# Kernel tuning notes

Hardware: AMD Instinct MI355X
Metric: run time of the kernel (lower is better)

## Reference

```python
import jax, jax.numpy as jnp
import numpy as np

N_NODES = 50000
N_EDGES = 600000
N_GRAPHS = 64
N_LAYERS = 4
D = 128
BN_EPS = 1e-5


def setup_inputs() -> dict:
    key = jax.random.key(0)
    ks = jax.random.split(key, 12)
    inp = {
        'x_node': jax.random.randint(ks[0], (N_NODES, 1), 0, 119, dtype=jnp.int64) if jax.config.jax_enable_x64 else jax.random.randint(ks[0], (N_NODES, 1), 0, 119).astype(jnp.int32),
        'edge_index': jax.random.randint(ks[1], (2, N_EDGES), 0, N_NODES).astype(jnp.int32),
        'batch': jnp.sort(jax.random.randint(ks[2], (N_NODES,), 0, N_GRAPHS)).astype(jnp.int32),
        'emb_table': jax.random.normal(ks[3], (119, D), jnp.float32),
        'conv_w1': jax.random.normal(ks[4], (N_LAYERS, D, D), jnp.float32) * 0.05,
        'conv_b1': jnp.zeros((N_LAYERS, D), jnp.float32),
        'bn1_g': jnp.ones((N_LAYERS, D), jnp.float32),
        'bn1_b': jnp.zeros((N_LAYERS, D), jnp.float32),
        'conv_w2': jax.random.normal(ks[5], (N_LAYERS, D, D), jnp.float32) * 0.05,
        'conv_b2': jnp.zeros((N_LAYERS, D), jnp.float32),
        'bn2_g': jnp.ones((N_LAYERS, D), jnp.float32),
        'bn2_b': jnp.zeros((N_LAYERS, D), jnp.float32),
        'lin1_w': jax.random.normal(ks[6], (D, 2 * D), jnp.float32) * 0.05,
        'lin1_b': jnp.zeros((2 * D,), jnp.float32),
        'lin2_w': jax.random.normal(ks[7], (2 * D, 10), jnp.float32) * 0.05,
        'lin2_b': jnp.zeros((10,), jnp.float32),
    }
    return inp


def _bn(h, g, b):
    # BatchNorm1d over the node axis (training-mode batch statistics, biased var)
    mu = jnp.mean(h, axis=0, keepdims=True)
    var = jnp.mean((h - mu) ** 2, axis=0, keepdims=True)
    return (h - mu) * jax.lax.rsqrt(var + BN_EPS) * g + b


def reference(x_node, edge_index, batch, emb_table, conv_w1, conv_b1, bn1_g, bn1_b,
              conv_w2, conv_b2, bn2_g, bn2_b, lin1_w, lin1_b, lin2_w, lin2_b):
    x = emb_table[x_node[:, 0]]                      # [N, D] node embedding
    src, dst = edge_index[0], edge_index[1]          # j, i in the torch code
    eps = 0.0
    for l in range(N_LAYERS):
        msg = x[src]                                 # gather x_j, [E, D]
        agg = jax.ops.segment_sum(msg, dst, num_segments=N_NODES)  # scatter-add to targets
        h = agg + (1.0 + eps) * x
        h = jax.nn.relu(_bn(h @ conv_w1[l] + conv_b1[l], bn1_g[l], bn1_b[l]))
        h = jax.nn.relu(_bn(h @ conv_w2[l] + conv_b2[l], bn2_g[l], bn2_b[l]))
        x = h
    # jump_mode=None -> last layer; readout: per-graph mean pooling
    ones = jnp.ones((N_NODES,), x.dtype)
    counts = jax.ops.segment_sum(ones, batch, num_segments=N_GRAPHS)
    pooled = jax.ops.segment_sum(x, batch, num_segments=N_GRAPHS)
    pooled = pooled / jnp.maximum(counts, 1.0)[:, None]             # [B, D]
    out = jax.nn.relu(pooled @ lin1_w + lin1_b)
    return out @ lin2_w + lin2_b                     # [B, 10]
```

## Files before the change

kernel.cpp:

```cpp
#include <hip/hip_runtime.h>
#include <hip/hip_fp16.h>

#define N_NODES 50000
#define N_EDGES 600000
#define N_GRAPHS 64
#define N_LAYERS 4
#define D 128
#define BN_EPS 1e-5f

#define SCAN_NB 49
#define GB 782

#define EMB_NB 6250
#define ZERO_NB 14
#define RPK_NB 8

typedef __attribute__((ext_vector_type(8))) short short8;
typedef __attribute__((ext_vector_type(8))) _Float16 half8;
typedef __attribute__((ext_vector_type(4))) float f32x4;

#define WLO_SCALE 2048.0f
#define WLO_INV (1.0f / 2048.0f)

__device__ __forceinline__ float half_bits_to_f32(short b) {
  union { unsigned short u; __half h; } cv;
  cv.u = (unsigned short)b;
  return __half2float(cv.h);
}
__device__ __forceinline__ unsigned short f32_to_half_bits(float f) {
  union { __half h; unsigned short u; } cv;
  cv.h = __float2half(f);
  return cv.u;
}

__global__ __launch_bounds__(256) void setup_kernel(const int* __restrict__ idx,
    const float* __restrict__ emb, __half* __restrict__ xh,
    int* __restrict__ counts, const float* __restrict__ cw1,
    const float* __restrict__ cw2, unsigned short* __restrict__ Wh,
    unsigned short* __restrict__ Wl) {
  int bb = blockIdx.x;
  int t = threadIdx.x;
  if (bb < EMB_NB) {
    int tid = bb * 256 + t;
    if (tid >= N_NODES * 32) return;
    int n = tid >> 5, c4 = tid & 31;
    int e = idx[n];
    float4 v = ((const float4*)emb)[(size_t)e * 32 + c4];
    __half2 a = __float22half2_rn(make_float2(v.x, v.y));
    __half2 b = __float22half2_rn(make_float2(v.z, v.w));
    ((__half2*)xh)[(size_t)tid * 2] = a;
    ((__half2*)xh)[(size_t)tid * 2 + 1] = b;
  } else if (bb < EMB_NB + ZERO_NB) {
    int tid = (bb - EMB_NB) * 256 + t;
    for (int i = tid; i < N_NODES; i += ZERO_NB * 256) counts[i] = 0;
  } else {
    int b = bb - (EMB_NB + ZERO_NB);
    int l = b >> 1, which = b & 1;
    const float* Wm = (which ? cw2 : cw1) + (size_t)l * D * D;
    unsigned short* outh = Wh + (size_t)b * D * D;
    unsigned short* outl = Wl + (size_t)b * D * D;
    for (int T = t; T < 2048; T += 256) {
      int ks = T >> 9, ct = (T >> 6) & 7, lane = T & 63;
      int kbase = ks * 32 + ((lane >> 4) << 3);
      int c = ct * 16 + (lane & 15);
      unsigned short hs[8], ls[8];
#pragma unroll
      for (int e = 0; e < 8; ++e) {
        float v = Wm[(size_t)(kbase + e) * D + c];
        __half hh = __float2half_rn(v);
        float rem = v - __half2float(hh);
        __half hl = __float2half_rn(rem * WLO_SCALE);
        union { __half h; unsigned short u; } c1, c2;
        c1.h = hh; c2.h = hl;
        hs[e] = c1.u;
        ls[e] = c2.u;
      }
      *(ushort4*)(outh + (size_t)T * 8)     = *(ushort4*)&hs[0];
      *(ushort4*)(outh + (size_t)T * 8 + 4) = *(ushort4*)&hs[4];
      *(ushort4*)(outl + (size_t)T * 8)     = *(ushort4*)&ls[0];
      *(ushort4*)(outl + (size_t)T * 8 + 4) = *(ushort4*)&ls[4];
    }
  }
}

__global__ __launch_bounds__(256) void count_kernel(const int* __restrict__ dst,
    int* __restrict__ counts) {
  int e = blockIdx.x * 256 + threadIdx.x;
  if (e < N_EDGES) atomicAdd(&counts[dst[e]], 1);
}

__global__ __launch_bounds__(256) void scan_block_kernel(const int* __restrict__ counts,
    int* __restrict__ offsets, int* __restrict__ partials) {
  __shared__ int s[256];
  int t = threadIdx.x;
  int base = blockIdx.x * 1024 + t * 4;
  int v[4];
#pragma unroll
  for (int i = 0; i < 4; ++i) v[i] = (base + i < N_NODES) ? counts[base + i] : 0;
  int tsum = v[0] + v[1] + v[2] + v[3];
  s[t] = tsum;
  __syncthreads();
  for (int off = 1; off < 256; off <<= 1) {
    int add = (t >= off) ? s[t - off] : 0;
    __syncthreads();
    s[t] += add;
    __syncthreads();
  }
  int run = s[t] - tsum;
#pragma unroll
  for (int i = 0; i < 4; ++i) {
    if (base + i < N_NODES) offsets[base + i] = run;
    run += v[i];
  }
  if (t == 255) partials[blockIdx.x] = s[255];
}

__global__ __launch_bounds__(256) void add_offsets_kernel(int* __restrict__ offsets,
    const int* __restrict__ partials, int* __restrict__ cursor) {
  __shared__ int pre[SCAN_NB];
  int t = threadIdx.x;
  if (t < SCAN_NB) pre[t] = partials[t];
  __syncthreads();
  if (t == 0) {
    int run = 0;
    for (int b = 0; b < SCAN_NB; ++b) { int v = pre[b]; pre[b] = run; run += v; }
  }
  __syncthreads();
  int i = blockIdx.x * 256 + t;
  if (i < N_NODES) {
    int o = offsets[i] + pre[i >> 10];
    offsets[i] = o;
    cursor[i] = o;
  }
  if (blockIdx.x == 0 && t == 0) offsets[N_NODES] = N_EDGES;
}

__global__ __launch_bounds__(256) void fill_csr_kernel(const int* __restrict__ src,
    const int* __restrict__ dst, int* __restrict__ cursor, int* __restrict__ col) {
  int e = blockIdx.x * 256 + threadIdx.x;
  if (e < N_EDGES) {
    int d = dst[e];
    int p = atomicAdd(&cursor[d], 1);
    col[p] = src[e];
  }
}

template <bool TRANS>
__global__ __launch_bounds__(256) void agg_kernel(const __half* __restrict__ xh,
    const int* __restrict__ offsets, const int* __restrict__ col,
    const float* __restrict__ scale, const float* __restrict__ shift,
    __half* __restrict__ h) {
  int node = blockIdx.x * 4 + (threadIdx.x >> 6);
  int lane = threadIdx.x & 63;
  float2 scl, shl;
  if (TRANS) {
    scl = ((const float2*)scale)[lane];
    shl = ((const float2*)shift)[lane];
  }
  const __half2* x2 = (const __half2*)xh;
  float2 self = __half22float2(x2[(size_t)node * 64 + lane]);
  float2 acc;
  if (TRANS) {
    acc.x = fmaxf(fmaf(self.x, scl.x, shl.x), 0.f);
    acc.y = fmaxf(fmaf(self.y, scl.y, shl.y), 0.f);
  } else {
    acc = self;
  }
  int beg = offsets[node], end = offsets[node + 1];
  for (int e = beg; e < end; e += 8) {
    int idx[8];
    bool val[8];
#pragma unroll
    for (int j = 0; j < 8; ++j) {
      val[j] = (e + j) < end;
      idx[j] = val[j] ? (e + j) : e;
    }
    int sidx[8];
#pragma unroll
    for (int j = 0; j < 8; ++j) sidx[j] = col[idx[j]];
    float2 ff[8];
#pragma unroll
    for (int j = 0; j < 8; ++j) ff[j] = __half22float2(x2[(size_t)sidx[j] * 64 + lane]);
#pragma unroll
    for (int j = 0; j < 8; ++j) {
      float2 v = ff[j];
      if (TRANS) {
        v.x = fmaxf(fmaf(v.x, scl.x, shl.x), 0.f);
        v.y = fmaxf(fmaf(v.y, scl.y, shl.y), 0.f);
      }
      if (val[j]) {
        acc.x += v.x;
        acc.y += v.y;
      }
    }
  }
  ((__half2*)h)[(size_t)node * 64 + lane] = __float22half2_rn(acc);
}

template <bool TRANS>
__global__ __launch_bounds__(256) void gemm_f16_kernel(
    const __half* __restrict__ A, const unsigned short* __restrict__ Wh,
    const unsigned short* __restrict__ Wl, const float* __restrict__ bias,
    const float* __restrict__ scale, const float* __restrict__ shift,
    __half* __restrict__ Y, float* __restrict__ ps, float* __restrict__ pq) {
  __shared__ unsigned short AL[64][136];
  int t = threadIdx.x;
  int row0 = blockIdx.x * 64;
  int lane = t & 63;
  int wv = t >> 6;

#pragma unroll
  for (int i = 0; i < 4; ++i) {
    int s = i * 256 + t;
    int r = s >> 4, c8 = s & 15;
    int row = row0 + r;
    short8 v = {0, 0, 0, 0, 0, 0, 0, 0};
    if (row < N_NODES) v = *(const short8*)(A + (size_t)row * D + c8 * 8);
    if (TRANS) {
      float4 sc0 = ((const float4*)scale)[c8 * 2];
      float4 sc1 = ((const float4*)scale)[c8 * 2 + 1];
      float4 sh0 = ((const float4*)shift)[c8 * 2];
      float4 sh1 = ((const float4*)shift)[c8 * 2 + 1];
      float scv[8] = {sc0.x, sc0.y, sc0.z, sc0.w, sc1.x, sc1.y, sc1.z, sc1.w};
      float shv[8] = {sh0.x, sh0.y, sh0.z, sh0.w, sh1.x, sh1.y, sh1.z, sh1.w};
      short8 o;
#pragma unroll
      for (int j = 0; j < 8; ++j) {
        float f = fmaxf(fmaf(half_bits_to_f32(v[j]), scv[j], shv[j]), 0.f);
        o[j] = (short)f32_to_half_bits(f);
      }
      v = o;
    }
    *(short8*)&AL[r][c8 * 8] = v;
  }
  __syncthreads();

  f32x4 acch[4][2], accl[4][2];
#pragma unroll
  for (int rt = 0; rt < 4; ++rt)
#pragma unroll
    for (int c = 0; c < 2; ++c) {
      acch[rt][c] = (f32x4){0.f, 0.f, 0.f, 0.f};
      accl[rt][c] = (f32x4){0.f, 0.f, 0.f, 0.f};
    }

  int arow_lo = lane & 15;
  int kgrp = (lane >> 4) * 8;
#pragma unroll
  for (int ks = 0; ks < 4; ++ks) {
    size_t wbase = ((size_t)(ks * 8 + wv * 2) * 64 + lane) * 8;
    half8 wh0 = __builtin_bit_cast(half8, *(const short8*)(Wh + wbase));
    half8 wl0 = __builtin_bit_cast(half8, *(const short8*)(Wl + wbase));
    half8 wh1 = __builtin_bit_cast(half8, *(const short8*)(Wh + wbase + 512));
    half8 wl1 = __builtin_bit_cast(half8, *(const short8*)(Wl + wbase + 512));
#pragma unroll
    for (int rt = 0; rt < 4; ++rt) {
      half8 av = __builtin_bit_cast(half8,
          *(const short8*)&AL[rt * 16 + arow_lo][ks * 32 + kgrp]);
      acch[rt][0] = __builtin_amdgcn_mfma_f32_16x16x32_f16(av, wh0, acch[rt][0], 0, 0, 0);
      accl[rt][0] = __builtin_amdgcn_mfma_f32_16x16x32_f16(av, wl0, accl[rt][0], 0, 0, 0);
      acch[rt][1] = __builtin_amdgcn_mfma_f32_16x16x32_f16(av, wh1, acch[rt][1], 0, 0, 0);
      accl[rt][1] = __builtin_amdgcn_mfma_f32_16x16x32_f16(av, wl1, accl[rt][1], 0, 0, 0);
    }
  }

  __syncthreads();

  int rsub = (lane >> 4) << 2;
  int cl = lane & 15;
#pragma unroll
  for (int cti = 0; cti < 2; ++cti) {
    int c = wv * 32 + cti * 16 + cl;
    float b = bias[c];
    float s = 0.f, q = 0.f;
#pragma unroll
    for (int rt = 0; rt < 4; ++rt) {
#pragma unroll
      for (int r = 0; r < 4; ++r) {
        int rl = rt * 16 + rsub + r;
        float y = fmaf(accl[rt][cti][r], WLO_INV, acch[rt][cti][r]) + b;
        ((__half*)&AL[rl][0])[c] = __float2half(y);
        if (row0 + rl < N_NODES) {
          s += y;
          q += y * y;
        }
      }
    }
    s += __shfl_xor(s, 16, 64);
    s += __shfl_xor(s, 32, 64);
    q += __shfl_xor(q, 16, 64);
    q += __shfl_xor(q, 32, 64);
    if (lane < 16) {
      ps[(size_t)blockIdx.x * 128 + c] = s;
      pq[(size_t)blockIdx.x * 128 + c] = q;
    }
  }
  __syncthreads();
#pragma unroll
  for (int i = 0; i < 4; ++i) {
    int s = i * 256 + t;
    int r = s >> 4, c8 = s & 15;
    int row = row0 + r;
    if (row < N_NODES) {
      ushort4 a = *(ushort4*)&AL[r][c8 * 8];
      ushort4 b = *(ushort4*)&AL[r][c8 * 8 + 4];
      *(ushort4*)((unsigned short*)Y + (size_t)row * D + c8 * 8)     = a;
      *(ushort4*)((unsigned short*)Y + (size_t)row * D + c8 * 8 + 4) = b;
    }
  }
}

__global__ __launch_bounds__(256) void finalize_kernel(const float* __restrict__ ps,
    const float* __restrict__ pq, const float* __restrict__ g, const float* __restrict__ b,
    float* __restrict__ scale, float* __restrict__ shift) {
  int c = blockIdx.x;
  int t = threadIdx.x;
  float s = 0.f, q = 0.f;
  for (int i = t; i < GB; i += 256) {
    s += ps[(size_t)i * 128 + c];
    q += pq[(size_t)i * 128 + c];
  }
#pragma unroll
  for (int o = 1; o < 64; o <<= 1) {
    s += __shfl_xor(s, o, 64);
    q += __shfl_xor(q, o, 64);
  }
  __shared__ float rs[4], rq[4];
  if ((t & 63) == 0) { rs[t >> 6] = s; rq[t >> 6] = q; }
  __syncthreads();
  if (t == 0) {
    s = rs[0] + rs[1] + rs[2] + rs[3];
    q = rq[0] + rq[1] + rq[2] + rq[3];
    float mu = s * (1.0f / N_NODES);
    float var = fmaxf(q * (1.0f / N_NODES) - mu * mu, 0.f);
    float sc = g[c] * rsqrtf(var + BN_EPS);
    scale[c] = sc;
    shift[c] = fmaf(-mu, sc, b[c]);
  }
}

__device__ __forceinline__ int lower_bound_batch(const int* __restrict__ batch, int key) {
  int lo = 0, hi = N_NODES;
  while (lo < hi) {
    int mid = (lo + hi) >> 1;
    if (batch[mid] < key) lo = mid + 1; else hi = mid;
  }
  return lo;
}

__global__ __launch_bounds__(256) void pool_kernel(const __half* __restrict__ x,
    const int* __restrict__ batch, const float* __restrict__ scale,
    const float* __restrict__ shift, float* __restrict__ pp, float* __restrict__ gcnt) {
  int g = blockIdx.x, chunk = blockIdx.y;
  int lo = lower_bound_batch(batch, g);
  int hi = lower_bound_batch(batch, g + 1);
  int f = threadIdx.x & 127, sub = threadIdx.x >> 7;
  float sc = scale[f], sh = shift[f];
  int cnt = hi - lo;
  int per = (cnt + 7) >> 3;
  int s = lo + chunk * per;
  int e = min(s + per, hi);
  float acc = 0.f;
  for (int n = s + sub; n < e; n += 2)
    acc += fmaxf(fmaf(__half2float(x[(size_t)n * 128 + f]), sc, sh), 0.f);
  __shared__ float red[2][128];
  red[sub][f] = acc;
  __syncthreads();
  if (sub == 0) pp[((size_t)g * 8 + chunk) * 128 + f] = red[0][f] + red[1][f];
  if (threadIdx.x == 0 && chunk == 0) gcnt[g] = (float)cnt;
}

__global__ __launch_bounds__(256) void mlp_kernel(const float* __restrict__ pp,
    const float* __restrict__ gcnt, const float* __restrict__ w1, const float* __restrict__ b1,
    const float* __restrict__ w2, const float* __restrict__ b2, float* __restrict__ out) {
  int g = blockIdx.x, t = threadIdx.x;
  __shared__ float p[128];
  __shared__ float hbuf[256];
  if (t < 128) {
    float s = 0.f;
#pragma unroll
    for (int c = 0; c < 8; ++c) s += pp[((size_t)g * 8 + c) * 128 + t];
    p[t] = s / fmaxf(gcnt[g], 1.0f);
  }
  __syncthreads();
  float acc = b1[t];
  for (int k = 0; k < 128; ++k) acc = fmaf(p[k], w1[k * 256 + t], acc);
  hbuf[t] = fmaxf(acc, 0.f);
  __syncthreads();
  if (t < 10) {
    float o = b2[t];
    for (int k = 0; k < 256; ++k) o = fmaf(hbuf[k], w2[k * 10 + t], o);
    out[g * 10 + t] = o;
  }
}

extern "C" void kernel_launch(void* const* d_in, const int* in_sizes, int n_in,
                              void* d_out, int out_size, void* d_ws, size_t ws_size,
                              hipStream_t stream) {
  const int* x_node = (const int*)d_in[0];
  const int* eidx = (const int*)d_in[1];
  const int* batch = (const int*)d_in[2];
  const float* emb = (const float*)d_in[3];
  const float* cw1 = (const float*)d_in[4];
  const float* cb1 = (const float*)d_in[5];
  const float* bn1g = (const float*)d_in[6];
  const float* bn1b = (const float*)d_in[7];
  const float* cw2 = (const float*)d_in[8];
  const float* cb2 = (const float*)d_in[9];
  const float* bn2g = (const float*)d_in[10];
  const float* bn2b = (const float*)d_in[11];
  const float* l1w = (const float*)d_in[12];
  const float* l1b = (const float*)d_in[13];
  const float* l2w = (const float*)d_in[14];
  const float* l2b = (const float*)d_in[15];
  float* out = (float*)d_out;

  char* ws = (char*)d_ws;
  size_t off = 0;
  auto carve = [&](size_t bytes) -> void* {
    void* p = ws + off;
    off += (bytes + 255) & ~(size_t)255;
    return p;
  };
  __half* xh   = (__half*)carve((size_t)N_NODES * D * 2);
  __half* abuf = (__half*)carve((size_t)N_NODES * D * 2);
  __half* ybuf = (__half*)carve((size_t)N_NODES * D * 2);
  __half* zbuf = (__half*)carve((size_t)N_NODES * D * 2);
  int* counts = (int*)carve((size_t)N_NODES * 4);
  int* offsets = (int*)carve((size_t)(N_NODES + 1) * 4);
  int* cursor = (int*)carve((size_t)N_NODES * 4);
  int* col = (int*)carve((size_t)N_EDGES * 4);
  int* partials = (int*)carve(64 * 4);
  float* part_s = (float*)carve((size_t)GB * 128 * 4);
  float* part_q = (float*)carve((size_t)GB * 128 * 4);
  float* scaleb = (float*)carve(8 * 128 * 4);
  float* shiftb = (float*)carve(8 * 128 * 4);
  float* pp = (float*)carve(64 * 8 * 128 * 4);
  float* gcnt = (float*)carve(64 * 4);
  unsigned short* Whb = (unsigned short*)carve((size_t)8 * D * D * 2);
  unsigned short* Wlb = (unsigned short*)carve((size_t)8 * D * D * 2);
  (void)ws_size;
  (void)in_sizes;
  (void)n_in;
  (void)out_size;

  const int* srcp = eidx;
  const int* dstp = eidx + N_EDGES;

  setup_kernel<<<EMB_NB + ZERO_NB + RPK_NB, 256, 0, stream>>>(
      x_node, emb, xh, counts, cw1, cw2, Whb, Wlb);
  count_kernel<<<(N_EDGES + 255) / 256, 256, 0, stream>>>(dstp, counts);
  scan_block_kernel<<<SCAN_NB, 256, 0, stream>>>(counts, offsets, partials);
  add_offsets_kernel<<<(N_NODES + 255) / 256, 256, 0, stream>>>(offsets, partials, cursor);
  fill_csr_kernel<<<(N_EDGES + 255) / 256, 256, 0, stream>>>(srcp, dstp, cursor, col);

  for (int l = 0; l < N_LAYERS; ++l) {
    float* sc1 = scaleb + (l * 2) * 128;
    float* sh1 = shiftb + (l * 2) * 128;
    float* sc2 = scaleb + (l * 2 + 1) * 128;
    float* sh2 = shiftb + (l * 2 + 1) * 128;
    const float* scp = scaleb + (l * 2 - 1) * 128;
    const float* shp = shiftb + (l * 2 - 1) * 128;
    const unsigned short* W1h = Whb + (size_t)(l * 2) * D * D;
    const unsigned short* W1l = Wlb + (size_t)(l * 2) * D * D;
    const unsigned short* W2h = Whb + (size_t)(l * 2 + 1) * D * D;
    const unsigned short* W2l = Wlb + (size_t)(l * 2 + 1) * D * D;

    if (l == 0)
      agg_kernel<false><<<12500, 256, 0, stream>>>(xh, offsets, col, nullptr, nullptr, abuf);
    else
      agg_kernel<true><<<12500, 256, 0, stream>>>(zbuf, offsets, col, scp, shp, abuf);
    gemm_f16_kernel<false><<<GB, 256, 0, stream>>>(abuf, W1h, W1l, cb1 + l * D,
                                                   nullptr, nullptr, ybuf, part_s, part_q);
    finalize_kernel<<<128, 256, 0, stream>>>(part_s, part_q, bn1g + l * D, bn1b + l * D,
                                             sc1, sh1);
    gemm_f16_kernel<true><<<GB, 256, 0, stream>>>(ybuf, W2h, W2l, cb2 + l * D,
                                                  sc1, sh1, zbuf, part_s, part_q);
    finalize_kernel<<<128, 256, 0, stream>>>(part_s, part_q, bn2g + l * D, bn2b + l * D,
                                             sc2, sh2);
  }

  pool_kernel<<<dim3(64, 8), 256, 0, stream>>>(zbuf, batch,
      scaleb + 7 * 128, shiftb + 7 * 128, pp, gcnt);
  mlp_kernel<<<64, 256, 0, stream>>>(pp, gcnt, l1w, l1b, l2w, l2b, out);
}
```

Before: 344.6 us.

## Enlarge GEMM tile to 128 rows with 8 waves each owning 16 columns

The dense layer GEMM now works on 128-row tiles with 512 threads per block. Each of the 8 waves computes one 16-column strip across all 8 row subtiles, where before 4 waves each computed two strips over 4 subtiles. This halves the grid and the number of BN partial sums that finalize has to reduce, and each weight fragment is reused across more rows. The cost is fewer blocks for a 50k-row problem (391 on a large GPU), more LDS per block, and possibly lower occupancy.

```diff
diff --git a/kernel.cpp b/kernel.cpp
--- a/kernel.cpp
+++ b/kernel.cpp
@@ -9,7 +9,7 @@
 #define BN_EPS 1e-5f
 
 #define SCAN_NB 49
-#define GB 782
+#define GB 391
 
 #define EMB_NB 6250
 #define ZERO_NB 14
@@ -198,20 +198,20 @@
 }
 
 template <bool TRANS>
-__global__ __launch_bounds__(256) void gemm_f16_kernel(
+__global__ __launch_bounds__(512) void gemm_f16_kernel(
     const __half* __restrict__ A, const unsigned short* __restrict__ Wh,
     const unsigned short* __restrict__ Wl, const float* __restrict__ bias,
     const float* __restrict__ scale, const float* __restrict__ shift,
     __half* __restrict__ Y, float* __restrict__ ps, float* __restrict__ pq) {
-  __shared__ unsigned short AL[64][136];
+  __shared__ unsigned short AL[128][136];
   int t = threadIdx.x;
-  int row0 = blockIdx.x * 64;
+  int row0 = blockIdx.x * 128;
   int lane = t & 63;
   int wv = t >> 6;
 
 #pragma unroll
   for (int i = 0; i < 4; ++i) {
-    int s = i * 256 + t;
+    int s = i * 512 + t;
     int r = s >> 4, c8 = s & 15;
     int row = row0 + r;
     short8 v = {0, 0, 0, 0, 0, 0, 0, 0};
@@ -235,32 +235,26 @@
   }
   __syncthreads();
 
-  f32x4 acch[4][2], accl[4][2];
-#pragma unroll
-  for (int rt = 0; rt < 4; ++rt)
-#pragma unroll
-    for (int c = 0; c < 2; ++c) {
-      acch[rt][c] = (f32x4){0.f, 0.f, 0.f, 0.f};
-      accl[rt][c] = (f32x4){0.f, 0.f, 0.f, 0.f};
-    }
+  f32x4 acch[8], accl[8];
+#pragma unroll
+  for (int rt = 0; rt < 8; ++rt) {
+    acch[rt] = (f32x4){0.f, 0.f, 0.f, 0.f};
+    accl[rt] = (f32x4){0.f, 0.f, 0.f, 0.f};
+  }
 
   int arow_lo = lane & 15;
   int kgrp = (lane >> 4) * 8;
 #pragma unroll
   for (int ks = 0; ks < 4; ++ks) {
-    size_t wbase = ((size_t)(ks * 8 + wv * 2) * 64 + lane) * 8;
-    half8 wh0 = __builtin_bit_cast(half8, *(const short8*)(Wh + wbase));
-    half8 wl0 = __builtin_bit_cast(half8, *(const short8*)(Wl + wbase));
-    half8 wh1 = __builtin_bit_cast(half8, *(const short8*)(Wh + wbase + 512));
-    half8 wl1 = __builtin_bit_cast(half8, *(const short8*)(Wl + wbase + 512));
-#pragma unroll
-    for (int rt = 0; rt < 4; ++rt) {
+    size_t wbase = ((size_t)(ks * 8 + wv) * 64 + lane) * 8;
+    half8 wh = __builtin_bit_cast(half8, *(const short8*)(Wh + wbase));
+    half8 wl = __builtin_bit_cast(half8, *(const short8*)(Wl + wbase));
+#pragma unroll
+    for (int rt = 0; rt < 8; ++rt) {
       half8 av = __builtin_bit_cast(half8,
           *(const short8*)&AL[rt * 16 + arow_lo][ks * 32 + kgrp]);
-      acch[rt][0] = __builtin_amdgcn_mfma_f32_16x16x32_f16(av, wh0, acch[rt][0], 0, 0, 0);
-      accl[rt][0] = __builtin_amdgcn_mfma_f32_16x16x32_f16(av, wl0, accl[rt][0], 0, 0, 0);
-      acch[rt][1] = __builtin_amdgcn_mfma_f32_16x16x32_f16(av, wh1, acch[rt][1], 0, 0, 0);
-      accl[rt][1] = __builtin_amdgcn_mfma_f32_16x16x32_f16(av, wl1, accl[rt][1], 0, 0, 0);
+      acch[rt] = __builtin_amdgcn_mfma_f32_16x16x32_f16(av, wh, acch[rt], 0, 0, 0);
+      accl[rt] = __builtin_amdgcn_mfma_f32_16x16x32_f16(av, wl, accl[rt], 0, 0, 0);
     }
   }
 
@@ -268,17 +262,16 @@
 
   int rsub = (lane >> 4) << 2;
   int cl = lane & 15;
-#pragma unroll
-  for (int cti = 0; cti < 2; ++cti) {
-    int c = wv * 32 + cti * 16 + cl;
+  {
+    int c = wv * 16 + cl;
     float b = bias[c];
     float s = 0.f, q = 0.f;
 #pragma unroll
-    for (int rt = 0; rt < 4; ++rt) {
+    for (int rt = 0; rt < 8; ++rt) {
 #pragma unroll
       for (int r = 0; r < 4; ++r) {
         int rl = rt * 16 + rsub + r;
-        float y = fmaf(accl[rt][cti][r], WLO_INV, acch[rt][cti][r]) + b;
+        float y = fmaf(accl[rt][r], WLO_INV, acch[rt][r]) + b;
         ((__half*)&AL[rl][0])[c] = __float2half(y);
         if (row0 + rl < N_NODES) {
           s += y;
@@ -298,7 +291,7 @@
   __syncthreads();
 #pragma unroll
   for (int i = 0; i < 4; ++i) {
-    int s = i * 256 + t;
+    int s = i * 512 + t;
     int r = s >> 4, c8 = s & 15;
     int row = row0 + r;
     if (row < N_NODES) {
@@ -470,11 +463,11 @@
       agg_kernel<false><<<12500, 256, 0, stream>>>(xh, offsets, col, nullptr, nullptr, abuf);
     else
       agg_kernel<true><<<12500, 256, 0, stream>>>(zbuf, offsets, col, scp, shp, abuf);
-    gemm_f16_kernel<false><<<GB, 256, 0, stream>>>(abuf, W1h, W1l, cb1 + l * D,
+    gemm_f16_kernel<false><<<GB, 512, 0, stream>>>(abuf, W1h, W1l, cb1 + l * D,
                                                    nullptr, nullptr, ybuf, part_s, part_q);
     finalize_kernel<<<128, 256, 0, stream>>>(part_s, part_q, bn1g + l * D, bn1b + l * D,
                                              sc1, sh1);
-    gemm_f16_kernel<true><<<GB, 256, 0, stream>>>(ybuf, W2h, W2l, cb2 + l * D,
+    gemm_f16_kernel<true><<<GB, 512, 0, stream>>>(ybuf, W2h, W2l, cb2 + l * D,
                                                   sc1, sh1, zbuf, part_s, part_q);
     finalize_kernel<<<128, 256, 0, stream>>>(part_s, part_q, bn2g + l * D, bn2b + l * D,
                                              sc2, sh2);
```

Result: no change. 351.4 us (+2.0%).

## Reduce BN stats via bucketed atomics and fold first finalize into GEMM

Applied to the files above, without the earlier changes.

The GEMM epilogue now atomically adds its per-column partial sums into 32 buckets instead of writing per-block partials. The first BN finalize is folded into the prologue of the second GEMM, and the remaining finalize shrinks to a single 128-thread block reading 32 buckets. This removes one kernel launch per layer and shrinks the partial-reduction traffic. In exchange it adds atomic contention on the buckets and makes the summation order nondeterministic.

```diff
diff --git a/kernel.cpp b/kernel.cpp
--- a/kernel.cpp
+++ b/kernel.cpp
@@ -10,6 +10,7 @@
 
 #define SCAN_NB 49
 #define GB 782
+#define NBUCKET 32
 
 #define EMB_NB 6250
 #define ZERO_NB 14
@@ -35,9 +36,9 @@
 
 __global__ __launch_bounds__(256) void setup_kernel(const int* __restrict__ idx,
     const float* __restrict__ emb, __half* __restrict__ xh,
-    int* __restrict__ counts, const float* __restrict__ cw1,
-    const float* __restrict__ cw2, unsigned short* __restrict__ Wh,
-    unsigned short* __restrict__ Wl) {
+    int* __restrict__ counts, float* __restrict__ buckets,
+    const float* __restrict__ cw1, const float* __restrict__ cw2,
+    unsigned short* __restrict__ Wh, unsigned short* __restrict__ Wl) {
   int bb = blockIdx.x;
   int t = threadIdx.x;
   if (bb < EMB_NB) {
@@ -53,6 +54,7 @@
   } else if (bb < EMB_NB + ZERO_NB) {
     int tid = (bb - EMB_NB) * 256 + t;
     for (int i = tid; i < N_NODES; i += ZERO_NB * 256) counts[i] = 0;
+    for (int i = tid; i < 16 * NBUCKET * 128; i += ZERO_NB * 256) buckets[i] = 0.f;
   } else {
     int b = bb - (EMB_NB + ZERO_NB);
     int l = b >> 1, which = b & 1;
@@ -197,17 +199,36 @@
   ((__half2*)h)[(size_t)node * 64 + lane] = __float22half2_rn(acc);
 }
 
-template <bool TRANS>
+template <bool FIN_IN>
 __global__ __launch_bounds__(256) void gemm_f16_kernel(
     const __half* __restrict__ A, const unsigned short* __restrict__ Wh,
     const unsigned short* __restrict__ Wl, const float* __restrict__ bias,
-    const float* __restrict__ scale, const float* __restrict__ shift,
-    __half* __restrict__ Y, float* __restrict__ ps, float* __restrict__ pq) {
+    const float* __restrict__ ibs, const float* __restrict__ ibq,
+    const float* __restrict__ bng, const float* __restrict__ bnb,
+    __half* __restrict__ Y, float* __restrict__ obs, float* __restrict__ obq) {
   __shared__ unsigned short AL[64][136];
+  __shared__ float scL[128], shL[128];
   int t = threadIdx.x;
   int row0 = blockIdx.x * 64;
   int lane = t & 63;
   int wv = t >> 6;
+
+  if (FIN_IN) {
+    if (t < 128) {
+      float s = 0.f, q = 0.f;
+#pragma unroll
+      for (int i = 0; i < NBUCKET; ++i) {
+        s += ibs[i * 128 + t];
+        q += ibq[i * 128 + t];
+      }
+      float mu = s * (1.0f / N_NODES);
+      float var = fmaxf(q * (1.0f / N_NODES) - mu * mu, 0.f);
+      float sc = bng[t] * rsqrtf(var + BN_EPS);
+      scL[t] = sc;
+      shL[t] = fmaf(-mu, sc, bnb[t]);
+    }
+    __syncthreads();
+  }
 
 #pragma unroll
   for (int i = 0; i < 4; ++i) {
@@ -216,11 +237,11 @@
     int row = row0 + r;
     short8 v = {0, 0, 0, 0, 0, 0, 0, 0};
     if (row < N_NODES) v = *(const short8*)(A + (size_t)row * D + c8 * 8);
-    if (TRANS) {
-      float4 sc0 = ((const float4*)scale)[c8 * 2];
-      float4 sc1 = ((const float4*)scale)[c8 * 2 + 1];
-      float4 sh0 = ((const float4*)shift)[c8 * 2];
-      float4 sh1 = ((const float4*)shift)[c8 * 2 + 1];
+    if (FIN_IN) {
+      float4 sc0 = *(const float4*)&scL[c8 * 8];
+      float4 sc1 = *(const float4*)&scL[c8 * 8 + 4];
+      float4 sh0 = *(const float4*)&shL[c8 * 8];
+      float4 sh1 = *(const float4*)&shL[c8 * 8 + 4];
       float scv[8] = {sc0.x, sc0.y, sc0.z, sc0.w, sc1.x, sc1.y, sc1.z, sc1.w};
       float shv[8] = {sh0.x, sh0.y, sh0.z, sh0.w, sh1.x, sh1.y, sh1.z, sh1.w};
       short8 o;
@@ -268,6 +289,7 @@
 
   int rsub = (lane >> 4) << 2;
   int cl = lane & 15;
+  int bkt = (blockIdx.x & (NBUCKET - 1)) * 128;
 #pragma unroll
   for (int cti = 0; cti < 2; ++cti) {
     int c = wv * 32 + cti * 16 + cl;
@@ -291,8 +313,8 @@
     q += __shfl_xor(q, 16, 64);
     q += __shfl_xor(q, 32, 64);
     if (lane < 16) {
-      ps[(size_t)blockIdx.x * 128 + c] = s;
-      pq[(size_t)blockIdx.x * 128 + c] = q;
+      atomicAdd(&obs[bkt + c], s);
+      atomicAdd(&obq[bkt + c], q);
     }
   }
   __syncthreads();
@@ -310,33 +332,21 @@
   }
 }
 
-__global__ __launch_bounds__(256) void finalize_kernel(const float* __restrict__ ps,
-    const float* __restrict__ pq, const float* __restrict__ g, const float* __restrict__ b,
+__global__ __launch_bounds__(128) void finalize_kernel(const float* __restrict__ bs,
+    const float* __restrict__ bq, const float* __restrict__ g, const float* __restrict__ b,
     float* __restrict__ scale, float* __restrict__ shift) {
-  int c = blockIdx.x;
-  int t = threadIdx.x;
+  int c = threadIdx.x;
   float s = 0.f, q = 0.f;
-  for (int i = t; i < GB; i += 256) {
-    s += ps[(size_t)i * 128 + c];
-    q += pq[(size_t)i * 128 + c];
-  }
-#pragma unroll
-  for (int o = 1; o < 64; o <<= 1) {
-    s += __shfl_xor(s, o, 64);
-    q += __shfl_xor(q, o, 64);
-  }
-  __shared__ float rs[4], rq[4];
-  if ((t & 63) == 0) { rs[t >> 6] = s; rq[t >> 6] = q; }
-  __syncthreads();
-  if (t == 0) {
-    s = rs[0] + rs[1] + rs[2] + rs[3];
-    q = rq[0] + rq[1] + rq[2] + rq[3];
-    float mu = s * (1.0f / N_NODES);
-    float var = fmaxf(q * (1.0f / N_NODES) - mu * mu, 0.f);
-    float sc = g[c] * rsqrtf(var + BN_EPS);
-    scale[c] = sc;
-    shift[c] = fmaf(-mu, sc, b[c]);
-  }
+#pragma unroll
+  for (int i = 0; i < NBUCKET; ++i) {
+    s += bs[i * 128 + c];
+    q += bq[i * 128 + c];
+  }
+  float mu = s * (1.0f / N_NODES);
+  float var = fmaxf(q * (1.0f / N_NODES) - mu * mu, 0.f);
+  float sc = g[c] * rsqrtf(var + BN_EPS);
+  scale[c] = sc;
+  shift[c] = fmaf(-mu, sc, b[c]);
 }
 
 __device__ __forceinline__ int lower_bound_batch(const int* __restrict__ batch, int key) {
@@ -431,10 +441,9 @@
   int* cursor = (int*)carve((size_t)N_NODES * 4);
   int* col = (int*)carve((size_t)N_EDGES * 4);
   int* partials = (int*)carve(64 * 4);
-  float* part_s = (float*)carve((size_t)GB * 128 * 4);
-  float* part_q = (float*)carve((size_t)GB * 128 * 4);
-  float* scaleb = (float*)carve(8 * 128 * 4);
-  float* shiftb = (float*)carve(8 * 128 * 4);
+  float* buckets = (float*)carve((size_t)16 * NBUCKET * 128 * 4);
+  float* scaleb = (float*)carve(4 * 128 * 4);
+  float* shiftb = (float*)carve(4 * 128 * 4);
   float* pp = (float*)carve(64 * 8 * 128 * 4);
   float* gcnt = (float*)carve(64 * 4);
   unsigned short* Whb = (unsigned short*)carve((size_t)8 * D * D * 2);
@@ -448,19 +457,22 @@
   const int* dstp = eidx + N_EDGES;
 
   setup_kernel<<<EMB_NB + ZERO_NB + RPK_NB, 256, 0, stream>>>(
-      x_node, emb, xh, counts, cw1, cw2, Whb, Wlb);
+      x_node, emb, xh, counts, buckets, cw1, cw2, Whb, Wlb);
   count_kernel<<<(N_EDGES + 255) / 256, 256, 0, stream>>>(dstp, counts);
   scan_block_kernel<<<SCAN_NB, 256, 0, stream>>>(counts, offsets, partials);
   add_offsets_kernel<<<(N_NODES + 255) / 256, 256, 0, stream>>>(offsets, partials, cursor);
   fill_csr_kernel<<<(N_EDGES + 255) / 256, 256, 0, stream>>>(srcp, dstp, cursor, col);
 
+  const size_t BSZ = (size_t)NBUCKET * 128;
   for (int l = 0; l < N_LAYERS; ++l) {
-    float* sc1 = scaleb + (l * 2) * 128;
-    float* sh1 = shiftb + (l * 2) * 128;
-    float* sc2 = scaleb + (l * 2 + 1) * 128;
-    float* sh2 = shiftb + (l * 2 + 1) * 128;
-    const float* scp = scaleb + (l * 2 - 1) * 128;
-    const float* shp = shiftb + (l * 2 - 1) * 128;
+    float* b1s = buckets + (l * 4 + 0) * BSZ;
+    float* b1q = buckets + (l * 4 + 1) * BSZ;
+    float* b2s = buckets + (l * 4 + 2) * BSZ;
+    float* b2q = buckets + (l * 4 + 3) * BSZ;
+    float* sc2 = scaleb + l * 128;
+    float* sh2 = shiftb + l * 128;
+    const float* scp = scaleb + (l - 1) * 128;
+    const float* shp = shiftb + (l - 1) * 128;
     const unsigned short* W1h = Whb + (size_t)(l * 2) * D * D;
     const unsigned short* W1l = Wlb + (size_t)(l * 2) * D * D;
     const unsigned short* W2h = Whb + (size_t)(l * 2 + 1) * D * D;
@@ -471,16 +483,13 @@
     else
       agg_kernel<true><<<12500, 256, 0, stream>>>(zbuf, offsets, col, scp, shp, abuf);
     gemm_f16_kernel<false><<<GB, 256, 0, stream>>>(abuf, W1h, W1l, cb1 + l * D,
-                                                   nullptr, nullptr, ybuf, part_s, part_q);
-    finalize_kernel<<<128, 256, 0, stream>>>(part_s, part_q, bn1g + l * D, bn1b + l * D,
-                                             sc1, sh1);
+        nullptr, nullptr, nullptr, nullptr, ybuf, b1s, b1q);
     gemm_f16_kernel<true><<<GB, 256, 0, stream>>>(ybuf, W2h, W2l, cb2 + l * D,
-                                                  sc1, sh1, zbuf, part_s, part_q);
-    finalize_kernel<<<128, 256, 0, stream>>>(part_s, part_q, bn2g + l * D, bn2b + l * D,
-                                             sc2, sh2);
+        b1s, b1q, bn1g + l * D, bn1b + l * D, zbuf, b2s, b2q);
+    finalize_kernel<<<1, 128, 0, stream>>>(b2s, b2q, bn2g + l * D, bn2b + l * D, sc2, sh2);
   }
 
   pool_kernel<<<dim3(64, 8), 256, 0, stream>>>(zbuf, batch,
-      scaleb + 7 * 128, shiftb + 7 * 128, pp, gcnt);
+      scaleb + 3 * 128, shiftb + 3 * 128, pp, gcnt);
   mlp_kernel<<<64, 256, 0, stream>>>(pp, gcnt, l1w, l1b, l2w, l2b, out);
 }
```

Result: faster. 330.3 us (-4.1%).
